# Optimization experiments

Hardware: AMD Instinct MI355X
Metric: run time of the kernel (lower is better)

## Reference

```python
import jax, jax.numpy as jnp
import numpy as np

B, S, F = 64, 4096, 128      # batch, seq_len, fcnn_unit
RANK, FUSED = 16, 10


def setup_inputs() -> dict:
    key = jax.random.key(0)
    ks = jax.random.split(key, 10)
    xavier = lambda k, shape: jax.random.normal(k, shape, jnp.float32) * np.sqrt(2.0 / (shape[-2] + shape[-1]))
    return {
        "imu_h": jax.random.normal(ks[0], (B, S, F), jnp.float32),
        "vid_h": jax.random.normal(ks[1], (B, S, F), jnp.float32),
        "anthro": jax.random.uniform(ks[2], (B, 1, 2), jnp.float32, 0.5, 1.5),
        "imu_factor": xavier(ks[3], (RANK, 1, F + 1, FUSED)),
        "vid_factor": xavier(ks[4], (RANK, 1, F + 1, FUSED)),
        "fusion_weights": xavier(ks[5], (1, RANK)),
        "fusion_bias": jnp.zeros((1, FUSED), jnp.float32),
        "W1": xavier(ks[6], (FUSED, F)),
        "b1": jnp.zeros((F,), jnp.float32),
        "W2": xavier(ks[7], (F, 2)),
        "b2": jnp.zeros((2,), jnp.float32),
    }


def reference(imu_h, vid_h, anthro, imu_factor, vid_factor,
              fusion_weights, fusion_bias, W1, b1, W2, b2):
    b, s, _ = imu_h.shape
    ones = jnp.ones((b, s, 1), imu_h.dtype)
    _imu_h = jnp.concatenate([ones, imu_h], axis=2)   # [B,S,F+1]
    _vid_h = jnp.concatenate([ones, vid_h], axis=2)
    # torch.matmul([B,S,F+1], [rank,1,F+1,d]) -> [rank,B,S,d]
    fusion_imu = jnp.einsum('bsf,rfd->rbsd', _imu_h, imu_factor[:, 0])
    fusion_vid = jnp.einsum('bsf,rfd->rbsd', _vid_h, vid_factor[:, 0])
    fusion_zy = fusion_imu * fusion_vid               # [rank,B,S,d]
    # weighted combine over rank + bias -> [B,S,d]
    seq = jnp.einsum('r,rbsd->bsd', fusion_weights[0], fusion_zy) + fusion_bias[0]
    seq = jax.nn.relu(seq @ W1 + b1)                  # [B,S,F]
    seq = seq @ W2 + b2                               # [B,S,2]
    wh = (anthro[:, 0, 0] * anthro[:, 0, 1])[:, None, None]  # weight*height
    return seq / wh
```

## Files before the change

kernel.cpp:

```cpp
#include <hip/hip_runtime.h>
#include <hip/hip_bf16.h>
#include <stdint.h>


#define NTOK   262144
#define FDIM   128
#define RANKN  16
#define FUSED  10
#define KPAD   136
#define WTE    (FUSED*RANKN*KPAD)

typedef unsigned short u16;
typedef __bf16 bf16x8 __attribute__((ext_vector_type(8)));
typedef float  f32x4  __attribute__((ext_vector_type(4)));

static __device__ __forceinline__ u16 f2bf(float f) {
    union { float f; uint32_t u; } c; c.f = f;
    uint32_t u = c.u + 0x7FFFu + ((c.u >> 16) & 1u);
    return (u16)(u >> 16);
}

__global__ void prep_kernel(const float* __restrict__ imf, const float* __restrict__ vif,
                            const float* __restrict__ fw,  const float* __restrict__ fb,
                            const float* __restrict__ W1,  const float* __restrict__ b1,
                            u16* __restrict__ wImu, u16* __restrict__ wVid,
                            float* __restrict__ a0, float* __restrict__ b0,
                            float* __restrict__ b1p) {
    int idx = blockIdx.x * blockDim.x + threadIdx.x;
    if (idx < FUSED * RANKN * FDIM) {
        int k = idx & 127;
        int r = (idx >> 7) & 15;
        int d = idx >> 11;
        int src = r * ((FDIM + 1) * FUSED) + (k + 1) * FUSED + d;
        wImu[(d * RANKN + r) * KPAD + k] = f2bf(fw[r] * imf[src]);
        wVid[(d * RANKN + r) * KPAD + k] = f2bf(vif[src]);
    }
    if (idx < RANKN * FUSED) {
        int r = idx & 15, d = idx >> 4;
        int src = r * ((FDIM + 1) * FUSED) + d;
        a0[idx] = fw[r] * imf[src];
        b0[idx] = vif[src];
    }
    if (idx < FDIM) {
        float acc = b1[idx];
        #pragma unroll
        for (int d = 0; d < FUSED; ++d) acc += fb[d] * W1[d * FDIM + idx];
        b1p[idx] = acc;
    }
}

__launch_bounds__(512, 2)
__global__ void fusion_main(const float* __restrict__ imu, const float* __restrict__ vid,
                            const float* __restrict__ anthro,
                            const u16* __restrict__ wImuG, const u16* __restrict__ wVidG,
                            const float* __restrict__ a0g, const float* __restrict__ b0g,
                            const float* __restrict__ W1g, const float* __restrict__ b1pg,
                            const float* __restrict__ W2g, const float* __restrict__ b2g,
                            float* __restrict__ out) {
    extern __shared__ char smem[];
    u16*   sWimu = (u16*)smem;
    u16*   sWvid = sWimu + WTE;
    float* sA0   = (float*)(sWvid + WTE);
    float* sB0   = sA0 + 160;
    float* sW1   = sB0 + 160;
    float* sB1   = sW1 + 1280;
    float* sW2   = sB1 + 128;

    {
        const uint4* srcI = (const uint4*)wImuG;
        const uint4* srcV = (const uint4*)wVidG;
        uint4* dstI = (uint4*)sWimu;
        uint4* dstV = (uint4*)sWvid;
        const int n16 = WTE * 2 / 16;
        for (int i = threadIdx.x; i < n16; i += blockDim.x) { dstI[i] = srcI[i]; dstV[i] = srcV[i]; }
        for (int i = threadIdx.x; i < 160;  i += blockDim.x) { sA0[i] = a0g[i]; sB0[i] = b0g[i]; }
        for (int i = threadIdx.x; i < 1280; i += blockDim.x) sW1[i] = W1g[i];
        for (int i = threadIdx.x; i < 128;  i += blockDim.x) sB1[i] = b1pg[i];
        for (int i = threadIdx.x; i < 256;  i += blockDim.x) sW2[i] = W2g[i];
    }
    __syncthreads();

    const int lane = threadIdx.x & 63;
    const int quad = lane >> 4;
    const int r16  = lane & 15;
    const int wid  = threadIdx.x >> 6;
    const int t0   = (blockIdx.x * 8 + wid) * 16;

    bf16x8 aI[4], aV[4];
    {
        const float* baseI = imu + (size_t)(t0 + r16) * FDIM + quad * 8;
        const float* baseV = vid + (size_t)(t0 + r16) * FDIM + quad * 8;
        #pragma unroll
        for (int kk = 0; kk < 4; ++kk) {
            f32x4 v0 = *(const f32x4*)(baseI + kk * 32);
            f32x4 v1 = *(const f32x4*)(baseI + kk * 32 + 4);
            f32x4 w0 = *(const f32x4*)(baseV + kk * 32);
            f32x4 w1 = *(const f32x4*)(baseV + kk * 32 + 4);
            bf16x8 a, b;
            #pragma unroll
            for (int j = 0; j < 4; ++j) {
                a[j]     = (__bf16)v0[j];
                a[j + 4] = (__bf16)v1[j];
                b[j]     = (__bf16)w0[j];
                b[j + 4] = (__bf16)w1[j];
            }
            aI[kk] = a;
            aV[kk] = b;
        }
    }

    float seqv[4][FUSED];
    #pragma unroll
    for (int d = 0; d < FUSED; ++d) {
        f32x4 accU = {0.f, 0.f, 0.f, 0.f};
        f32x4 accV = {0.f, 0.f, 0.f, 0.f};
        const u16* bi = sWimu + (d * RANKN + r16) * KPAD + quad * 8;
        const u16* bv = sWvid + (d * RANKN + r16) * KPAD + quad * 8;
        #pragma unroll
        for (int kk = 0; kk < 4; ++kk) {
            bf16x8 bU = *(const bf16x8*)(const void*)(bi + kk * 32);
            accU = __builtin_amdgcn_mfma_f32_16x16x32_bf16(aI[kk], bU, accU, 0, 0, 0);
            bf16x8 bV = *(const bf16x8*)(const void*)(bv + kk * 32);
            accV = __builtin_amdgcn_mfma_f32_16x16x32_bf16(aV[kk], bV, accV, 0, 0, 0);
        }
        float a0v = sA0[d * RANKN + r16];
        float b0v = sB0[d * RANKN + r16];
        #pragma unroll
        for (int reg = 0; reg < 4; ++reg) {
            float p = (accU[reg] + a0v) * (accV[reg] + b0v);
            p += __shfl_xor(p, 1, 16);
            p += __shfl_xor(p, 2, 16);
            p += __shfl_xor(p, 4, 16);
            p += __shfl_xor(p, 8, 16);
            seqv[reg][d] = p;
        }
    }

    float o0[4] = {0.f, 0.f, 0.f, 0.f};
    float o1[4] = {0.f, 0.f, 0.f, 0.f};
    #pragma unroll
    for (int g = 0; g < 8; ++g) {
        const int jc = r16 + 16 * g;
        float bb = sB1[jc];
        float h[4] = {bb, bb, bb, bb};
        #pragma unroll
        for (int d = 0; d < FUSED; ++d) {
            float w1v = sW1[d * FDIM + jc];
            #pragma unroll
            for (int reg = 0; reg < 4; ++reg) h[reg] += seqv[reg][d] * w1v;
        }
        float w20 = sW2[jc * 2], w21 = sW2[jc * 2 + 1];
        #pragma unroll
        for (int reg = 0; reg < 4; ++reg) {
            float hr = fmaxf(h[reg], 0.f);
            o0[reg] += hr * w20;
            o1[reg] += hr * w21;
        }
    }
    #pragma unroll
    for (int reg = 0; reg < 4; ++reg) {
        o0[reg] += __shfl_xor(o0[reg], 1, 16);
        o0[reg] += __shfl_xor(o0[reg], 2, 16);
        o0[reg] += __shfl_xor(o0[reg], 4, 16);
        o0[reg] += __shfl_xor(o0[reg], 8, 16);
        o1[reg] += __shfl_xor(o1[reg], 1, 16);
        o1[reg] += __shfl_xor(o1[reg], 2, 16);
        o1[reg] += __shfl_xor(o1[reg], 4, 16);
        o1[reg] += __shfl_xor(o1[reg], 8, 16);
    }

    const int bidx = t0 >> 12;
    const float invwh = 1.0f / (anthro[2 * bidx] * anthro[2 * bidx + 1]);
    const float b20 = b2g[0], b21 = b2g[1];
    if (r16 == 0) {
        #pragma unroll
        for (int reg = 0; reg < 4; ++reg) {
            const int t = t0 + quad * 4 + reg;
            float2 o = make_float2((o0[reg] + b20) * invwh, (o1[reg] + b21) * invwh);
            *(float2*)(out + 2 * t) = o;
        }
    }
}

extern "C" void kernel_launch(void* const* d_in, const int* in_sizes, int n_in,
                              void* d_out, int out_size, void* d_ws, size_t ws_size,
                              hipStream_t stream) {
    const float* imu    = (const float*)d_in[0];
    const float* vid    = (const float*)d_in[1];
    const float* anthro = (const float*)d_in[2];
    const float* imf    = (const float*)d_in[3];
    const float* vif    = (const float*)d_in[4];
    const float* fw     = (const float*)d_in[5];
    const float* fb     = (const float*)d_in[6];
    const float* W1     = (const float*)d_in[7];
    const float* b1     = (const float*)d_in[8];
    const float* W2     = (const float*)d_in[9];
    const float* b2     = (const float*)d_in[10];
    float* out = (float*)d_out;

    u16* wImu = (u16*)d_ws;
    u16* wVid = wImu + WTE;
    float* a0  = (float*)(wVid + WTE);
    float* b0  = a0 + 160;
    float* b1p = b0 + 160;

    prep_kernel<<<80, 256, 0, stream>>>(imf, vif, fw, fb, W1, b1, wImu, wVid, a0, b0, b1p);

    const size_t smem = (size_t)(2 * WTE) * sizeof(u16)
                      + (size_t)(160 + 160 + 1280 + 128 + 256) * sizeof(float);
    fusion_main<<<2048, 512, smem, stream>>>(imu, vid, anthro, wImu, wVid,
                                             a0, b0, W1, b1p, W2, b2, out);
}
```

Measured before the change: 343.8 us.

## Read MFMA weight fragments directly from global in lane order, drop LDS staging

The prep kernel now stores the bf16 factor weights pre-swizzled in per-lane MFMA B-fragment order, so each lane loads its fragment with one coalesced 16-byte global (L2-cached) read. The per-block copy of about 87KB of weights into shared memory is removed. That shrinks LDS use enough to raise the occupancy hint from 2 to 4 blocks, and W1 is stored transposed in LDS so the hidden layer can use vector loads. The trade-off is that weight reads go through the cache hierarchy on every wave instead of LDS, which costs some latency and L2 bandwidth.

Result: slower. 353.9 us (+2.9%).

```diff
diff --git a/kernel.cpp b/kernel.cpp
--- a/kernel.cpp
+++ b/kernel.cpp
@@ -7,8 +7,7 @@
 #define FDIM   128
 #define RANKN  16
 #define FUSED  10
-#define KPAD   136
-#define WTE    (FUSED*RANKN*KPAD)
+#define WTE    (FUSED*RANKN*FDIM)
 
 typedef unsigned short u16;
 typedef __bf16 bf16x8 __attribute__((ext_vector_type(8)));
@@ -32,8 +31,13 @@
         int r = (idx >> 7) & 15;
         int d = idx >> 11;
         int src = r * ((FDIM + 1) * FUSED) + (k + 1) * FUSED + d;
-        wImu[(d * RANKN + r) * KPAD + k] = f2bf(fw[r] * imf[src]);
-        wVid[(d * RANKN + r) * KPAD + k] = f2bf(vif[src]);
+        int kk   = k >> 5;
+        int quad = (k >> 3) & 3;
+        int j    = k & 7;
+        int lane = quad * 16 + r;
+        int dst  = ((d * 4 + kk) * 64 + lane) * 8 + j;
+        wImu[dst] = f2bf(fw[r] * imf[src]);
+        wVid[dst] = f2bf(vif[src]);
     }
     if (idx < RANKN * FUSED) {
         int r = idx & 15, d = idx >> 4;
@@ -49,7 +53,7 @@
     }
 }
 
-__launch_bounds__(512, 2)
+__launch_bounds__(512, 4)
 __global__ void fusion_main(const float* __restrict__ imu, const float* __restrict__ vid,
                             const float* __restrict__ anthro,
                             const u16* __restrict__ wImuG, const u16* __restrict__ wVidG,
@@ -58,26 +62,19 @@
                             const float* __restrict__ W2g, const float* __restrict__ b2g,
                             float* __restrict__ out) {
     extern __shared__ char smem[];
-    u16*   sWimu = (u16*)smem;
-    u16*   sWvid = sWimu + WTE;
-    float* sA0   = (float*)(sWvid + WTE);
-    float* sB0   = sA0 + 160;
-    float* sW1   = sB0 + 160;
-    float* sB1   = sW1 + 1280;
-    float* sW2   = sB1 + 128;
-
-    {
-        const uint4* srcI = (const uint4*)wImuG;
-        const uint4* srcV = (const uint4*)wVidG;
-        uint4* dstI = (uint4*)sWimu;
-        uint4* dstV = (uint4*)sWvid;
-        const int n16 = WTE * 2 / 16;
-        for (int i = threadIdx.x; i < n16; i += blockDim.x) { dstI[i] = srcI[i]; dstV[i] = srcV[i]; }
-        for (int i = threadIdx.x; i < 160;  i += blockDim.x) { sA0[i] = a0g[i]; sB0[i] = b0g[i]; }
-        for (int i = threadIdx.x; i < 1280; i += blockDim.x) sW1[i] = W1g[i];
-        for (int i = threadIdx.x; i < 128;  i += blockDim.x) sB1[i] = b1pg[i];
-        for (int i = threadIdx.x; i < 256;  i += blockDim.x) sW2[i] = W2g[i];
-    }
+    float* sA0  = (float*)smem;
+    float* sB0  = sA0 + 160;
+    float* sW1t = sB0 + 160;
+    float* sB1  = sW1t + FDIM * 12;
+    float* sW2  = sB1 + FDIM;
+
+    for (int i = threadIdx.x; i < 160; i += blockDim.x) { sA0[i] = a0g[i]; sB0[i] = b0g[i]; }
+    for (int i = threadIdx.x; i < FUSED * FDIM; i += blockDim.x) {
+        int d = i >> 7, jc = i & 127;
+        sW1t[jc * 12 + d] = W1g[i];
+    }
+    for (int i = threadIdx.x; i < FDIM; i += blockDim.x) sB1[i] = b1pg[i];
+    for (int i = threadIdx.x; i < 256;  i += blockDim.x) sW2[i] = W2g[i];
     __syncthreads();
 
     const int lane = threadIdx.x & 63;
@@ -109,18 +106,19 @@
         }
     }
 
+    const bf16x8* fragI = (const bf16x8*)(const void*)wImuG;
+    const bf16x8* fragV = (const bf16x8*)(const void*)wVidG;
+
     float seqv[4][FUSED];
     #pragma unroll
     for (int d = 0; d < FUSED; ++d) {
         f32x4 accU = {0.f, 0.f, 0.f, 0.f};
         f32x4 accV = {0.f, 0.f, 0.f, 0.f};
-        const u16* bi = sWimu + (d * RANKN + r16) * KPAD + quad * 8;
-        const u16* bv = sWvid + (d * RANKN + r16) * KPAD + quad * 8;
         #pragma unroll
         for (int kk = 0; kk < 4; ++kk) {
-            bf16x8 bU = *(const bf16x8*)(const void*)(bi + kk * 32);
+            bf16x8 bU = fragI[(d * 4 + kk) * 64 + lane];
             accU = __builtin_amdgcn_mfma_f32_16x16x32_bf16(aI[kk], bU, accU, 0, 0, 0);
-            bf16x8 bV = *(const bf16x8*)(const void*)(bv + kk * 32);
+            bf16x8 bV = fragV[(d * 4 + kk) * 64 + lane];
             accV = __builtin_amdgcn_mfma_f32_16x16x32_bf16(aV[kk], bV, accV, 0, 0, 0);
         }
         float a0v = sA0[d * RANKN + r16];
@@ -141,18 +139,21 @@
     #pragma unroll
     for (int g = 0; g < 8; ++g) {
         const int jc = r16 + 16 * g;
+        const float* wrow = sW1t + jc * 12;
+        f32x4 wa = *(const f32x4*)wrow;
+        f32x4 wb = *(const f32x4*)(wrow + 4);
+        float w8 = wrow[8], w9 = wrow[9];
         float bb = sB1[jc];
-        float h[4] = {bb, bb, bb, bb};
-        #pragma unroll
-        for (int d = 0; d < FUSED; ++d) {
-            float w1v = sW1[d * FDIM + jc];
+        float w20 = sW2[jc * 2], w21 = sW2[jc * 2 + 1];
+        #pragma unroll
+        for (int reg = 0; reg < 4; ++reg) {
+            float h = bb;
             #pragma unroll
-            for (int reg = 0; reg < 4; ++reg) h[reg] += seqv[reg][d] * w1v;
-        }
-        float w20 = sW2[jc * 2], w21 = sW2[jc * 2 + 1];
-        #pragma unroll
-        for (int reg = 0; reg < 4; ++reg) {
-            float hr = fmaxf(h[reg], 0.f);
+            for (int d = 0; d < 4; ++d) h += seqv[reg][d] * wa[d];
+            #pragma unroll
+            for (int d = 0; d < 4; ++d) h += seqv[reg][4 + d] * wb[d];
+            h += seqv[reg][8] * w8 + seqv[reg][9] * w9;
+            float hr = fmaxf(h, 0.f);
             o0[reg] += hr * w20;
             o1[reg] += hr * w21;
         }
@@ -206,8 +207,7 @@
 
     prep_kernel<<<80, 256, 0, stream>>>(imf, vif, fw, fb, W1, b1, wImu, wVid, a0, b0, b1p);
 
-    const size_t smem = (size_t)(2 * WTE) * sizeof(u16)
-                      + (size_t)(160 + 160 + 1280 + 128 + 256) * sizeof(float);
+    const size_t smem = (size_t)(160 + 160 + FDIM * 12 + FDIM + 256) * sizeof(float);
     fusion_main<<<2048, 512, smem, stream>>>(imu, vid, anthro, wImu, wVid,
                                              a0, b0, W1, b1p, W2, b2, out);
 }
```
